# Optimization experiments

Measured on AMD Instinct MI355X. Metric: run time of the kernel, lower is better.

## Reference

```python
import jax, jax.numpy as jnp
import numpy as np

SCALE_XY = 1.2           # yolo1 in Yolov4Head
OBJ_THRESH = 0.5         # b_o >= 0.5 gate in post_process
BOX_SCORE_THRESH = 0.05
NMS_THRESH = 0.7         # rpn_nms_thresh
MAX_DET = 300            # fixed capacity for jit-compatible NMS


def _decode(x, anchors):
    # x: [B, A*(5+C), H, W] -> boxes [B,H,W,A,4] (xyxy, normalized), obj logits, class logits
    b, c, h, w = x.shape
    a = anchors.shape[0]
    nc = c // a - 5
    out = x.reshape(b, a, 5 + nc, h, w).transpose(0, 3, 4, 1, 2)  # [B,H,W,A,5+C]
    cx = jnp.arange(w, dtype=x.dtype).reshape(1, 1, w, 1)
    cy = jnp.arange(h, dtype=x.dtype).reshape(1, h, 1, 1)
    xy = SCALE_XY * jax.nn.sigmoid(out[..., :2]) - 0.5 * (SCALE_XY - 1)
    bx = (xy[..., 0] + cx) / w
    by = (xy[..., 1] + cy) / h
    b_xy = jnp.stack([bx, by], axis=-1)
    b_wh = jnp.clip(jnp.exp(out[..., 2:4]) * anchors.reshape(1, 1, 1, a, 2), 0.0, 2.0)
    tl = b_xy - 0.5 * b_wh
    boxes = jnp.concatenate([tl, tl + b_wh], axis=-1)  # [B,H,W,A,4]
    return boxes, out[..., 4], out[..., 5:]


def _iou_one_vs_all(box, boxes):
    lt = jnp.maximum(box[:2], boxes[:, :2])
    rb = jnp.minimum(box[2:], boxes[:, 2:])
    wh = jnp.clip(rb - lt, 0.0)
    inter = wh[:, 0] * wh[:, 1]
    a1 = (box[2] - box[0]) * (box[3] - box[1])
    a2 = (boxes[:, 2] - boxes[:, 0]) * (boxes[:, 3] - boxes[:, 1])
    return inter / (a1 + a2 - inter + 1e-9)


def _post_process_single(boxes, b_o, b_scores):
    # boxes [N,4], b_o [N], b_scores [N,C]; fixed-size equivalent of YoloLayer.post_process
    obj = jax.nn.sigmoid(b_o)
    cls = jax.nn.sigmoid(b_scores)
    boxes = jnp.clip(boxes, 0.0, 1.0)
    labels = jnp.argmax(cls, axis=-1)
    score = jnp.max(cls, axis=-1) * obj
    valid = (obj >= OBJ_THRESH) & (score >= BOX_SCORE_THRESH)
    masked = jnp.where(valid, score, -1.0)
    _, top_i = jax.lax.top_k(masked, MAX_DET)
    sel_boxes = boxes[top_i]
    sel_labels = labels[top_i]
    sel_valid = valid[top_i]
    sel_scores = jnp.where(sel_valid, score[top_i], 0.0)
    pos = jnp.arange(MAX_DET)

    def body(i, keep):
        iou = _iou_one_vs_all(sel_boxes[i], sel_boxes)
        suppress = (iou > NMS_THRESH) & keep[i] & (pos > i)
        return keep & (~suppress)

    keep = jax.lax.fori_loop(0, MAX_DET, body, sel_valid)
    return sel_boxes, sel_scores, sel_labels, keep


def setup_inputs() -> dict:
    key = jax.random.key(0)
    k1, _ = jax.random.split(key)
    x = jax.random.normal(k1, (32, 255, 76, 76), dtype=jnp.float32)
    anchors = jnp.array([[12.0, 16.0], [19.0, 36.0], [40.0, 28.0]], dtype=jnp.float32) / 608.0
    return {"x": x, "anchors": anchors}


def reference(x, anchors):
    boxes, b_o, b_s = _decode(x, anchors)
    b = x.shape[0]
    nc = b_s.shape[-1]
    boxes = boxes.reshape(b, -1, 4)
    b_o = b_o.reshape(b, -1)
    b_s = b_s.reshape(b, -1, nc)
    det_boxes, det_scores, det_labels, keep = jax.vmap(_post_process_single)(boxes, b_o, b_s)
    return det_boxes, det_scores, det_labels, keep
```

## Files before the change

kernel.cpp:

```cpp
#include <hip/hip_runtime.h>
#include <stdint.h>

#define BATCH   32
#define GRID_HW 5776
#define NA      3
#define NPB     (NA*GRID_HW)
#define NCLS    80
#define MAXDET  300
#define NBINS   4096
#define CANDN   512
#define T2      1024
#define CHUNK   17
#define NQ      (BATCH*NPB/4)
#define S4      (GRID_HW/4)
#define NPB4    (NPB/4)

__device__ __forceinline__ float sigf(float x){ return 1.0f/(1.0f + expf(-x)); }

__device__ __forceinline__ int binf(float v){
    if (v < 0.0f) return 0;
    int b = (int)(v * 4096.0f);
    return b > (NBINS-1) ? (NBINS-1) : b;
}

__device__ __forceinline__ unsigned int ordf(float v){
    unsigned int u = __float_as_uint(v);
    return (u & 0x80000000u) ? ~u : (u | 0x80000000u);
}

__global__ __launch_bounds__(256) void decode_kernel(const float* __restrict__ x,
                                                     float* __restrict__ wmsk,
                                                     int* __restrict__ wlab)
{
    int tid = blockIdx.x * 256 + threadIdx.x;
    if (tid >= NQ) return;
    int b   = tid / (NPB/4);
    int r   = tid - b * (NPB/4);
    int a   = r / S4;
    int hw4 = r - a * S4;

    const float4* p4 = (const float4*)(x + (size_t)(b * 255 + a * 85) * GRID_HW) + hw4;

    float4 tov = p4[4*S4];

    float bx0=-1.0f, bx1=-1.0f, bx2=-1.0f, bx3=-1.0f;
    int   l0=0, l1=0, l2=0, l3=0;
    const float4* pc = p4 + 5*S4;
    #pragma unroll 4
    for (int c = 0; c < NCLS; ++c){
        float4 v = pc[(size_t)c * S4];
        float s;
        s = sigf(v.x); if (s > bx0){ bx0 = s; l0 = c; }
        s = sigf(v.y); if (s > bx1){ bx1 = s; l1 = c; }
        s = sigf(v.z); if (s > bx2){ bx2 = s; l2 = c; }
        s = sigf(v.w); if (s > bx3){ bx3 = s; l3 = c; }
    }

    float to[4]    = {tov.x, tov.y, tov.z, tov.w};
    float bestv[4] = {bx0, bx1, bx2, bx3};
    int   bestl[4] = {l0, l1, l2, l3};

    #pragma unroll
    for (int j = 0; j < 4; ++j){
        float obj = sigf(to[j]);
        float score = bestv[j] * obj;
        bool valid = (obj >= 0.5f) && (score >= 0.05f);

        int m = 4*tid + j;
        wmsk[m] = valid ? score : -1.0f;
        wlab[m] = bestl[j];
    }
}

__global__ __launch_bounds__(T2) void postproc_kernel(const float* __restrict__ x,
                                                      const float* __restrict__ anchors,
                                                      const float* __restrict__ wmsk,
                                                      const int* __restrict__ wlab,
                                                      float* __restrict__ out)
{
    __shared__ unsigned int shist[NBINS];
    __shared__ unsigned int wsum[16];
    __shared__ unsigned long long scan64[T2];
    __shared__ unsigned long long cand[CANDN];
    __shared__ float sbx[MAXDET], sby[MAXDET], sbz[MAXDET], sbw2[MAXDET];
    __shared__ float ssc[MAXDET];
    __shared__ int   slab[MAXDET];
    __shared__ unsigned long long adj[MAXDET][5];
    __shared__ unsigned long long kmask[5];
    __shared__ int s_bin, s_cnt;

    int t = threadIdx.x;
    int b = blockIdx.x;
    int wid = t >> 6, lane = t & 63;
    const float* msk = wmsk + (size_t)b * NPB;
    const float4* msk4 = (const float4*)msk;

    for (int i = t; i < NBINS; i += T2) shist[i] = 0u;
    if (t == 0){ s_bin = -2; s_cnt = 0; }
    __syncthreads();
    for (int i4 = t; i4 < NPB4; i4 += T2){
        float4 v4 = msk4[i4];
        if (v4.x >= 0.0f) atomicAdd(&shist[binf(v4.x)], 1u);
        if (v4.y >= 0.0f) atomicAdd(&shist[binf(v4.y)], 1u);
        if (v4.z >= 0.0f) atomicAdd(&shist[binf(v4.z)], 1u);
        if (v4.w >= 0.0f) atomicAdd(&shist[binf(v4.w)], 1u);
    }
    __syncthreads();

    unsigned int cs = shist[4*t] + shist[4*t+1] + shist[4*t+2] + shist[4*t+3];
    unsigned int vI = cs;
    #pragma unroll
    for (int d = 1; d < 64; d <<= 1){
        unsigned int o = __shfl_up(vI, d);
        if (lane >= d) vI += o;
    }
    if (lane == 63) wsum[wid] = vI;
    __syncthreads();
    if (t < 16){
        unsigned int s = wsum[t];
        #pragma unroll
        for (int d = 1; d < 16; d <<= 1){
            unsigned int o = __shfl_up(s, d);
            if (t >= d) s += o;
        }
        wsum[t] = s;
    }
    __syncthreads();
    unsigned int S = vI + (wid ? wsum[wid-1] : 0u);
    unsigned int total = wsum[15];
    if (total >= MAXDET){
        unsigned int c = total - S;
        #pragma unroll
        for (int k = 3; k >= 0; --k){
            unsigned int cg = c + shist[4*t + k];
            if (c < MAXDET && cg >= MAXDET) s_bin = 4*t + k;
            c = cg;
        }
    }
    __syncthreads();
    int cb = s_bin;

    if (cb >= 0){
        for (int i4 = t; i4 < NPB4; i4 += T2){
            float4 v4 = msk4[i4];
            float vv[4] = {v4.x, v4.y, v4.z, v4.w};
            #pragma unroll
            for (int j = 0; j < 4; ++j){
                float v = vv[j];
                bool pred = (v >= 0.0f) && (binf(v) >= cb);
                unsigned long long bal = __ballot(pred);
                if (bal){
                    int cnt = __popcll(bal);
                    int leader = __ffsll((long long)bal) - 1;
                    int lbase = 0;
                    if (lane == leader) lbase = atomicAdd(&s_cnt, cnt);
                    int base = __shfl(lbase, leader);
                    if (pred){
                        int off = __popcll(bal & ((1ull << lane) - 1ull));
                        int pos = base + off;
                        if (pos < CANDN){
                            int m = 4*i4 + j;
                            int aidx = m / GRID_HW;
                            int hw   = m - aidx * GRID_HW;
                            unsigned int n = (unsigned int)(hw * 3 + aidx);
                            cand[pos] = ((unsigned long long)ordf(v) << 32) | (~n);
                        }
                    }
                }
            }
        }
    }
    __syncthreads();
    int cnum = s_cnt;
    bool exact = (cb >= 0) && (cnum <= CANDN);

    if (exact){
        for (int i = cnum + t; i < CANDN; i += T2) cand[i] = 0ull;
        __syncthreads();
        for (int k2 = 2; k2 <= CANDN; k2 <<= 1){
            for (int j = k2 >> 1; j > 0; j >>= 1){
                if (t < CANDN){
                    int ixj = t ^ j;
                    if (ixj > t){
                        unsigned long long a1 = cand[t], b1 = cand[ixj];
                        bool up = ((t & k2) == 0);
                        if ((a1 < b1) == up){ cand[t] = b1; cand[ixj] = a1; }
                    }
                }
                __syncthreads();
            }
        }
    } else {
        unsigned long long lk[CHUNK];
        int cstart = t * CHUNK;
        int ccnt = NPB - cstart; ccnt = ccnt < 0 ? 0 : (ccnt > CHUNK ? CHUNK : ccnt);
        for (int k = 0; k < CHUNK; ++k) lk[k] = 0ull;
        for (int k = 0; k < ccnt; ++k){
            int m = cstart + k;
            int aidx = m / GRID_HW;
            int hw   = m - aidx * GRID_HW;
            unsigned int n = (unsigned int)(hw * 3 + aidx);
            lk[k] = ((unsigned long long)ordf(msk[m]) << 32) | (~n);
        }
        for (int it = 0; it < MAXDET; ++it){
            unsigned long long lm = 0ull;
            for (int k = 0; k < CHUNK; ++k) lm = lk[k] > lm ? lk[k] : lm;
            scan64[t] = lm;
            __syncthreads();
            for (int s = T2 >> 1; s > 0; s >>= 1){
                if (t < s){ unsigned long long o = scan64[t+s]; if (o > scan64[t]) scan64[t] = o; }
                __syncthreads();
            }
            unsigned long long win = scan64[0];
            if (t == 0) cand[it] = win;
            for (int k = 0; k < CHUNK; ++k) if (lk[k] == win) lk[k] = 0ull;
            __syncthreads();
        }
        for (int i = MAXDET + t; i < CANDN; i += T2) cand[i] = 0ull;
        __syncthreads();
    }

    {
        bool valid = false;
        if (t < MAXDET){
            unsigned long long key = cand[t];
            unsigned int n = ~((unsigned int)key);
            int aidx = (int)(n % 3u);
            int hw   = (int)(n / 3u);
            int m    = aidx * GRID_HW + hw;
            float v  = msk[m];
            valid = v > -0.5f;

            int h = hw / 76;
            int w = hw - h * 76;
            const float* p = x + (size_t)(b * 255 + aidx * 85) * GRID_HW + hw;
            float tx = p[0];
            float ty = p[GRID_HW];
            float tw = p[2*GRID_HW];
            float th = p[3*GRID_HW];
            float aw = anchors[aidx*2], ah = anchors[aidx*2+1];

            float sx = 1.2f * sigf(tx) - 0.1f;
            float sy = 1.2f * sigf(ty) - 0.1f;
            float bxc = (sx + (float)w) / 76.0f;
            float byc = (sy + (float)h) / 76.0f;
            float bw = fminf(fmaxf(expf(tw)*aw, 0.0f), 2.0f);
            float bh = fminf(fmaxf(expf(th)*ah, 0.0f), 2.0f);
            float tlx = bxc - 0.5f*bw, tly = byc - 0.5f*bh;
            float brx = tlx + bw,      bry = tly + bh;

            sbx[t]  = fminf(fmaxf(tlx,0.0f),1.0f);
            sby[t]  = fminf(fmaxf(tly,0.0f),1.0f);
            sbz[t]  = fminf(fmaxf(brx,0.0f),1.0f);
            sbw2[t] = fminf(fmaxf(bry,0.0f),1.0f);
            ssc[t]  = valid ? v : 0.0f;
            slab[t] = wlab[(size_t)b * NPB + m];
        }
        if (wid < 5){
            unsigned long long bal = __ballot(valid);
            if (lane == 0) kmask[wid] = bal;
        }
    }
    __syncthreads();

    for (int task = wid; task < MAXDET*5; task += 16){
        int i  = task / 5;
        int w2 = task - i * 5;
        int j  = w2 * 64 + lane;
        int jc = j < MAXDET ? j : (MAXDET-1);
        float lx = fmaxf(sbx[i], sbx[jc]);
        float ly = fmaxf(sby[i], sby[jc]);
        float rx = fminf(sbz[i], sbz[jc]);
        float ry = fminf(sbw2[i], sbw2[jc]);
        float iw = fmaxf(rx - lx, 0.0f);
        float ih = fmaxf(ry - ly, 0.0f);
        float inter = iw * ih;
        float a1 = (sbz[i]-sbx[i]) * (sbw2[i]-sby[i]);
        float a2 = (sbz[jc]-sbx[jc]) * (sbw2[jc]-sby[jc]);
        float iou = inter / (a1 + a2 - inter + 1e-9f);
        bool pred = (j < MAXDET) && (j > i) && (iou > 0.7f);
        unsigned long long bal = __ballot(pred);
        if (lane == 0) adj[i][w2] = bal;
    }
    __syncthreads();

    if (t < 64){
        unsigned long long km0 = kmask[0], km1 = kmask[1], km2 = kmask[2],
                           km3 = kmask[3], km4 = kmask[4];
        unsigned long long c0 = adj[0][0], c1 = adj[0][1], c2 = adj[0][2],
                           c3 = adj[0][3], c4 = adj[0][4];
        #define NMS_BLK(B, LIM, KM)                                            \
        for (int i2 = 0; i2 < (LIM); ++i2){                                    \
            int i = (B)*64 + i2;                                               \
            unsigned long long n0=0ull,n1=0ull,n2=0ull,n3=0ull,n4=0ull;        \
            if (i + 1 < MAXDET){                                               \
                n0 = adj[i+1][0]; n1 = adj[i+1][1]; n2 = adj[i+1][2];          \
                n3 = adj[i+1][3]; n4 = adj[i+1][4];                            \
            }                                                                  \
            unsigned long long m2 = ((KM >> i2) & 1ull) ? ~0ull : 0ull;        \
            km0 &= ~(c0 & m2);                                                 \
            km1 &= ~(c1 & m2);                                                 \
            km2 &= ~(c2 & m2);                                                 \
            km3 &= ~(c3 & m2);                                                 \
            km4 &= ~(c4 & m2);                                                 \
            c0 = n0; c1 = n1; c2 = n2; c3 = n3; c4 = n4;                       \
        }
        NMS_BLK(0, 64, km0)
        NMS_BLK(1, 64, km1)
        NMS_BLK(2, 64, km2)
        NMS_BLK(3, 64, km3)
        NMS_BLK(4, 44, km4)
        #undef NMS_BLK
        if (t == 0){
            kmask[0] = km0; kmask[1] = km1; kmask[2] = km2;
            kmask[3] = km3; kmask[4] = km4;
        }
    }
    __syncthreads();

    if (t < MAXDET){
        float* ob = out + (size_t)b * (MAXDET*4) + (size_t)t * 4;
        ob[0] = sbx[t]; ob[1] = sby[t]; ob[2] = sbz[t]; ob[3] = sbw2[t];
        out[BATCH*MAXDET*4 + b*MAXDET + t] = ssc[t];
        out[BATCH*MAXDET*5 + b*MAXDET + t] = (float)slab[t];
        out[BATCH*MAXDET*6 + b*MAXDET + t] = ((kmask[t >> 6] >> (t & 63)) & 1ull) ? 1.0f : 0.0f;
    }
}

extern "C" void kernel_launch(void* const* d_in, const int* in_sizes, int n_in,
                              void* d_out, int out_size, void* d_ws, size_t ws_size,
                              hipStream_t stream)
{
    const float* x       = (const float*)d_in[0];
    const float* anchors = (const float*)d_in[1];
    float* out = (float*)d_out;

    char* ws = (char*)d_ws;
    float* wmsk = (float*)ws;
    int*   wlab = (int*)(ws + (size_t)BATCH*NPB*4);

    decode_kernel<<<(NQ + 255)/256, 256, 0, stream>>>(x, wmsk, wlab);
    postproc_kernel<<<BATCH, T2, 0, stream>>>(x, anchors, wmsk, wlab, out);
}
```

Measured before the change: 344.7 us.

## Build score histogram in decode and split candidate selection across blocks

```diff
diff --git a/kernel.cpp b/kernel.cpp
--- a/kernel.cpp
+++ b/kernel.cpp
@@ -14,6 +14,9 @@
 #define NQ      (BATCH*NPB/4)
 #define S4      (GRID_HW/4)
 #define NPB4    (NPB/4)
+#define SB      8
+#define SLICE4  542
+#define ZN      (BATCH*NBINS + BATCH)
 
 __device__ __forceinline__ float sigf(float x){ return 1.0f/(1.0f + expf(-x)); }
 
@@ -28,9 +31,16 @@
     return (u & 0x80000000u) ? ~u : (u | 0x80000000u);
 }
 
+__global__ void zero_kernel(unsigned int* __restrict__ g)
+{
+    int i = blockIdx.x * blockDim.x + threadIdx.x;
+    if (i < ZN) g[i] = 0u;
+}
+
 __global__ __launch_bounds__(256) void decode_kernel(const float* __restrict__ x,
                                                      float* __restrict__ wmsk,
-                                                     int* __restrict__ wlab)
+                                                     int* __restrict__ wlab,
+                                                     unsigned int* __restrict__ ghist)
 {
     int tid = blockIdx.x * 256 + threadIdx.x;
     if (tid >= NQ) return;
@@ -69,13 +79,103 @@
         int m = 4*tid + j;
         wmsk[m] = valid ? score : -1.0f;
         wlab[m] = bestl[j];
-    }
-}
-
-__global__ __launch_bounds__(T2) void postproc_kernel(const float* __restrict__ x,
+        if (valid) atomicAdd(&ghist[b * NBINS + binf(score)], 1u);
+    }
+}
+
+__global__ __launch_bounds__(T2) void select_kernel(const float* __restrict__ wmsk,
+                                                    const unsigned int* __restrict__ ghist,
+                                                    unsigned long long* __restrict__ gcand,
+                                                    unsigned int* __restrict__ gcnt)
+{
+    __shared__ unsigned int shist[NBINS];
+    __shared__ unsigned int wsum[16];
+    __shared__ int s_bin;
+
+    int t = threadIdx.x;
+    int blk = blockIdx.x;
+    int b  = blk >> 3;
+    int sb = blk & 7;
+    int wid = t >> 6, lane = t & 63;
+
+    for (int i = t; i < NBINS; i += T2) shist[i] = ghist[b * NBINS + i];
+    if (t == 0) s_bin = -2;
+    __syncthreads();
+
+    unsigned int cs = shist[4*t] + shist[4*t+1] + shist[4*t+2] + shist[4*t+3];
+    unsigned int vI = cs;
+    #pragma unroll
+    for (int d = 1; d < 64; d <<= 1){
+        unsigned int o = __shfl_up(vI, d);
+        if (lane >= d) vI += o;
+    }
+    if (lane == 63) wsum[wid] = vI;
+    __syncthreads();
+    if (t < 16){
+        unsigned int s = wsum[t];
+        #pragma unroll
+        for (int d = 1; d < 16; d <<= 1){
+            unsigned int o = __shfl_up(s, d);
+            if (t >= d) s += o;
+        }
+        wsum[t] = s;
+    }
+    __syncthreads();
+    unsigned int S = vI + (wid ? wsum[wid-1] : 0u);
+    unsigned int total = wsum[15];
+    if (total >= MAXDET){
+        unsigned int c = total - S;
+        #pragma unroll
+        for (int k = 3; k >= 0; --k){
+            unsigned int cg = c + shist[4*t + k];
+            if (c < MAXDET && cg >= MAXDET) s_bin = 4*t + k;
+            c = cg;
+        }
+    }
+    __syncthreads();
+    int cb = s_bin;
+    if (cb < 0) return;
+
+    const float4* msk4 = (const float4*)(wmsk + (size_t)b * NPB);
+    int i4lim = sb * SLICE4 + SLICE4; if (i4lim > NPB4) i4lim = NPB4;
+    for (int i4 = sb * SLICE4 + t; i4 < i4lim; i4 += T2){
+        float4 v4 = msk4[i4];
+        float vv[4] = {v4.x, v4.y, v4.z, v4.w};
+        #pragma unroll
+        for (int j = 0; j < 4; ++j){
+            float v = vv[j];
+            bool pred = (v >= 0.0f) && (binf(v) >= cb);
+            unsigned long long bal = __ballot(pred);
+            if (bal){
+                int cnt = __popcll(bal);
+                int leader = __ffsll((long long)bal) - 1;
+                int lbase = 0;
+                if (lane == leader) lbase = (int)atomicAdd(&gcnt[b], (unsigned int)cnt);
+                int base = __shfl(lbase, leader);
+                if (pred){
+                    int off = __popcll(bal & ((1ull << lane) - 1ull));
+                    int pos = base + off;
+                    if (pos < CANDN){
+                        int m = 4*i4 + j;
+                        int aidx = m / GRID_HW;
+                        int hw   = m - aidx * GRID_HW;
+                        unsigned int n = (unsigned int)(hw * 3 + aidx);
+                        gcand[(size_t)b * CANDN + pos] =
+                            ((unsigned long long)ordf(v) << 32) | (~n);
+                    }
+                }
+            }
+        }
+    }
+}
+
+__global__ __launch_bounds__(T2) void finalize_kernel(const float* __restrict__ x,
                                                       const float* __restrict__ anchors,
                                                       const float* __restrict__ wmsk,
                                                       const int* __restrict__ wlab,
+                                                      const unsigned int* __restrict__ ghist,
+                                                      const unsigned long long* __restrict__ gcand,
+                                                      const unsigned int* __restrict__ gcnt,
                                                       float* __restrict__ out)
 {
     __shared__ unsigned int shist[NBINS];
@@ -87,24 +187,15 @@
     __shared__ int   slab[MAXDET];
     __shared__ unsigned long long adj[MAXDET][5];
     __shared__ unsigned long long kmask[5];
-    __shared__ int s_bin, s_cnt;
+    __shared__ int s_bin;
 
     int t = threadIdx.x;
     int b = blockIdx.x;
     int wid = t >> 6, lane = t & 63;
     const float* msk = wmsk + (size_t)b * NPB;
-    const float4* msk4 = (const float4*)msk;
-
-    for (int i = t; i < NBINS; i += T2) shist[i] = 0u;
-    if (t == 0){ s_bin = -2; s_cnt = 0; }
-    __syncthreads();
-    for (int i4 = t; i4 < NPB4; i4 += T2){
-        float4 v4 = msk4[i4];
-        if (v4.x >= 0.0f) atomicAdd(&shist[binf(v4.x)], 1u);
-        if (v4.y >= 0.0f) atomicAdd(&shist[binf(v4.y)], 1u);
-        if (v4.z >= 0.0f) atomicAdd(&shist[binf(v4.z)], 1u);
-        if (v4.w >= 0.0f) atomicAdd(&shist[binf(v4.w)], 1u);
-    }
+
+    for (int i = t; i < NBINS; i += T2) shist[i] = ghist[b * NBINS + i];
+    if (t == 0) s_bin = -2;
     __syncthreads();
 
     unsigned int cs = shist[4*t] + shist[4*t+1] + shist[4*t+2] + shist[4*t+3];
@@ -139,43 +230,12 @@
     }
     __syncthreads();
     int cb = s_bin;
-
-    if (cb >= 0){
-        for (int i4 = t; i4 < NPB4; i4 += T2){
-            float4 v4 = msk4[i4];
-            float vv[4] = {v4.x, v4.y, v4.z, v4.w};
-            #pragma unroll
-            for (int j = 0; j < 4; ++j){
-                float v = vv[j];
-                bool pred = (v >= 0.0f) && (binf(v) >= cb);
-                unsigned long long bal = __ballot(pred);
-                if (bal){
-                    int cnt = __popcll(bal);
-                    int leader = __ffsll((long long)bal) - 1;
-                    int lbase = 0;
-                    if (lane == leader) lbase = atomicAdd(&s_cnt, cnt);
-                    int base = __shfl(lbase, leader);
-                    if (pred){
-                        int off = __popcll(bal & ((1ull << lane) - 1ull));
-                        int pos = base + off;
-                        if (pos < CANDN){
-                            int m = 4*i4 + j;
-                            int aidx = m / GRID_HW;
-                            int hw   = m - aidx * GRID_HW;
-                            unsigned int n = (unsigned int)(hw * 3 + aidx);
-                            cand[pos] = ((unsigned long long)ordf(v) << 32) | (~n);
-                        }
-                    }
-                }
-            }
-        }
-    }
-    __syncthreads();
-    int cnum = s_cnt;
+    int cnum = (int)gcnt[b];
     bool exact = (cb >= 0) && (cnum <= CANDN);
 
     if (exact){
-        for (int i = cnum + t; i < CANDN; i += T2) cand[i] = 0ull;
+        for (int i = t; i < CANDN; i += T2)
+            cand[i] = (i < cnum) ? gcand[(size_t)b * CANDN + i] : 0ull;
         __syncthreads();
         for (int k2 = 2; k2 <= CANDN; k2 <<= 1){
             for (int j = k2 >> 1; j > 0; j >>= 1){
@@ -336,9 +396,15 @@
     float* out = (float*)d_out;
 
     char* ws = (char*)d_ws;
-    float* wmsk = (float*)ws;
-    int*   wlab = (int*)(ws + (size_t)BATCH*NPB*4);
-
-    decode_kernel<<<(NQ + 255)/256, 256, 0, stream>>>(x, wmsk, wlab);
-    postproc_kernel<<<BATCH, T2, 0, stream>>>(x, anchors, wmsk, wlab, out);
-}
+    float*              wmsk  = (float*)ws;
+    int*                wlab  = (int*)  (ws + (size_t)BATCH*NPB*4);
+    unsigned int*       ghist = (unsigned int*)(ws + (size_t)BATCH*NPB*8);
+    unsigned int*       gcnt  = ghist + (size_t)BATCH*NBINS;
+    unsigned long long* gcand = (unsigned long long*)(ws + (size_t)BATCH*NPB*8
+                                                      + (size_t)BATCH*NBINS*4 + 128);
+
+    zero_kernel<<<(ZN + 255)/256, 256, 0, stream>>>(ghist);
+    decode_kernel<<<(NQ + 255)/256, 256, 0, stream>>>(x, wmsk, wlab, ghist);
+    select_kernel<<<BATCH*SB, T2, 0, stream>>>(wmsk, ghist, gcand, gcnt);
+    finalize_kernel<<<BATCH, T2, 0, stream>>>(x, anchors, wmsk, wlab, ghist, gcand, gcnt, out);
+}
```

Result: slower. 391.9 us (+13.7%).

## Fuse decode and postprocess into one kernel with last-block-done per batch

Applied to the files above, without the earlier changes.

```diff
diff --git a/kernel.cpp b/kernel.cpp
--- a/kernel.cpp
+++ b/kernel.cpp
@@ -14,6 +14,9 @@
 #define NQ      (BATCH*NPB/4)
 #define S4      (GRID_HW/4)
 #define NPB4    (NPB/4)
+#define QPB     (NPB/4)
+#define NBLK    256
+#define SLICE   542
 
 __device__ __forceinline__ float sigf(float x){ return 1.0f/(1.0f + expf(-x)); }
 
@@ -28,75 +31,33 @@
     return (u & 0x80000000u) ? ~u : (u | 0x80000000u);
 }
 
-__global__ __launch_bounds__(256) void decode_kernel(const float* __restrict__ x,
-                                                     float* __restrict__ wmsk,
-                                                     int* __restrict__ wlab)
+__global__ void zero_kernel(unsigned int* __restrict__ qdone)
 {
-    int tid = blockIdx.x * 256 + threadIdx.x;
-    if (tid >= NQ) return;
-    int b   = tid / (NPB/4);
-    int r   = tid - b * (NPB/4);
-    int a   = r / S4;
-    int hw4 = r - a * S4;
-
-    const float4* p4 = (const float4*)(x + (size_t)(b * 255 + a * 85) * GRID_HW) + hw4;
-
-    float4 tov = p4[4*S4];
-
-    float bx0=-1.0f, bx1=-1.0f, bx2=-1.0f, bx3=-1.0f;
-    int   l0=0, l1=0, l2=0, l3=0;
-    const float4* pc = p4 + 5*S4;
-    #pragma unroll 4
-    for (int c = 0; c < NCLS; ++c){
-        float4 v = pc[(size_t)c * S4];
-        float s;
-        s = sigf(v.x); if (s > bx0){ bx0 = s; l0 = c; }
-        s = sigf(v.y); if (s > bx1){ bx1 = s; l1 = c; }
-        s = sigf(v.z); if (s > bx2){ bx2 = s; l2 = c; }
-        s = sigf(v.w); if (s > bx3){ bx3 = s; l3 = c; }
-    }
-
-    float to[4]    = {tov.x, tov.y, tov.z, tov.w};
-    float bestv[4] = {bx0, bx1, bx2, bx3};
-    int   bestl[4] = {l0, l1, l2, l3};
-
-    #pragma unroll
-    for (int j = 0; j < 4; ++j){
-        float obj = sigf(to[j]);
-        float score = bestv[j] * obj;
-        bool valid = (obj >= 0.5f) && (score >= 0.05f);
-
-        int m = 4*tid + j;
-        wmsk[m] = valid ? score : -1.0f;
-        wlab[m] = bestl[j];
-    }
-}
-
-__global__ __launch_bounds__(T2) void postproc_kernel(const float* __restrict__ x,
-                                                      const float* __restrict__ anchors,
-                                                      const float* __restrict__ wmsk,
-                                                      const int* __restrict__ wlab,
-                                                      float* __restrict__ out)
+    int i = threadIdx.x;
+    if (i < BATCH) qdone[i] = 0u;
+}
+
+__device__ void postproc_batch(int b, int t,
+                               const float* __restrict__ x,
+                               const float* __restrict__ anchors,
+                               const float* __restrict__ wmsk,
+                               const int* __restrict__ wlab,
+                               float* __restrict__ out,
+                               unsigned int* shist, unsigned int* wsum,
+                               unsigned long long* scan64, unsigned long long* cand,
+                               float* sbx, float* sby, float* sbz, float* sbw2,
+                               float* ssc, int* slab,
+                               unsigned long long (*adj)[5], unsigned long long* kmask,
+                               int* s_bin, int* s_cnt)
 {
-    __shared__ unsigned int shist[NBINS];
-    __shared__ unsigned int wsum[16];
-    __shared__ unsigned long long scan64[T2];
-    __shared__ unsigned long long cand[CANDN];
-    __shared__ float sbx[MAXDET], sby[MAXDET], sbz[MAXDET], sbw2[MAXDET];
-    __shared__ float ssc[MAXDET];
-    __shared__ int   slab[MAXDET];
-    __shared__ unsigned long long adj[MAXDET][5];
-    __shared__ unsigned long long kmask[5];
-    __shared__ int s_bin, s_cnt;
-
-    int t = threadIdx.x;
-    int b = blockIdx.x;
     int wid = t >> 6, lane = t & 63;
     const float* msk = wmsk + (size_t)b * NPB;
     const float4* msk4 = (const float4*)msk;
 
+    __syncthreads();
+
     for (int i = t; i < NBINS; i += T2) shist[i] = 0u;
-    if (t == 0){ s_bin = -2; s_cnt = 0; }
+    if (t == 0){ *s_bin = -2; *s_cnt = 0; }
     __syncthreads();
     for (int i4 = t; i4 < NPB4; i4 += T2){
         float4 v4 = msk4[i4];
@@ -133,12 +94,12 @@
         #pragma unroll
         for (int k = 3; k >= 0; --k){
             unsigned int cg = c + shist[4*t + k];
-            if (c < MAXDET && cg >= MAXDET) s_bin = 4*t + k;
+            if (c < MAXDET && cg >= MAXDET) *s_bin = 4*t + k;
             c = cg;
         }
     }
     __syncthreads();
-    int cb = s_bin;
+    int cb = *s_bin;
 
     if (cb >= 0){
         for (int i4 = t; i4 < NPB4; i4 += T2){
@@ -153,7 +114,7 @@
                     int cnt = __popcll(bal);
                     int leader = __ffsll((long long)bal) - 1;
                     int lbase = 0;
-                    if (lane == leader) lbase = atomicAdd(&s_cnt, cnt);
+                    if (lane == leader) lbase = atomicAdd(s_cnt, cnt);
                     int base = __shfl(lbase, leader);
                     if (pred){
                         int off = __popcll(bal & ((1ull << lane) - 1ull));
@@ -171,7 +132,7 @@
         }
     }
     __syncthreads();
-    int cnum = s_cnt;
+    int cnum = *s_cnt;
     bool exact = (cb >= 0) && (cnum <= CANDN);
 
     if (exact){
@@ -327,6 +288,101 @@
     }
 }
 
+__global__ __launch_bounds__(T2) void fused_kernel(const float* __restrict__ x,
+                                                   const float* __restrict__ anchors,
+                                                   float* __restrict__ wmsk,
+                                                   int* __restrict__ wlab,
+                                                   unsigned int* __restrict__ qdone,
+                                                   float* __restrict__ out)
+{
+    __shared__ unsigned int shist[NBINS];
+    __shared__ unsigned int wsum[16];
+    __shared__ unsigned long long scan64[T2];
+    __shared__ unsigned long long cand[CANDN];
+    __shared__ float sbx[MAXDET], sby[MAXDET], sbz[MAXDET], sbw2[MAXDET];
+    __shared__ float ssc[MAXDET];
+    __shared__ int   slab[MAXDET];
+    __shared__ unsigned long long adj[MAXDET][5];
+    __shared__ unsigned long long kmask[5];
+    __shared__ int s_bin, s_cnt;
+    __shared__ int s_do[2];
+
+    int t   = threadIdx.x;
+    int blk = blockIdx.x;
+    int q0  = blk * SLICE;
+    int q1  = q0 + SLICE; if (q1 > NQ) q1 = NQ;
+
+    int q = q0 + t;
+    if (q < q1){
+        int b   = q / QPB;
+        int r   = q - b * QPB;
+        int a   = r / S4;
+        int hw4 = r - a * S4;
+
+        const float4* p4 = (const float4*)(x + (size_t)(b * 255 + a * 85) * GRID_HW) + hw4;
+
+        float4 tov = p4[4*S4];
+
+        float bx0=-1.0f, bx1=-1.0f, bx2=-1.0f, bx3=-1.0f;
+        int   l0=0, l1=0, l2=0, l3=0;
+        const float4* pc = p4 + 5*S4;
+        #pragma unroll 4
+        for (int c = 0; c < NCLS; ++c){
+            float4 v = pc[(size_t)c * S4];
+            float s;
+            s = sigf(v.x); if (s > bx0){ bx0 = s; l0 = c; }
+            s = sigf(v.y); if (s > bx1){ bx1 = s; l1 = c; }
+            s = sigf(v.z); if (s > bx2){ bx2 = s; l2 = c; }
+            s = sigf(v.w); if (s > bx3){ bx3 = s; l3 = c; }
+        }
+
+        float to[4]    = {tov.x, tov.y, tov.z, tov.w};
+        float bestv[4] = {bx0, bx1, bx2, bx3};
+        int   bestl[4] = {l0, l1, l2, l3};
+
+        #pragma unroll
+        for (int j = 0; j < 4; ++j){
+            float obj = sigf(to[j]);
+            float score = bestv[j] * obj;
+            bool valid = (obj >= 0.5f) && (score >= 0.05f);
+
+            int m = 4*q + j;
+            wmsk[m] = valid ? score : -1.0f;
+            wlab[m] = bestl[j];
+        }
+    }
+
+    __threadfence();
+    __syncthreads();
+    if (t == 0){
+        s_do[0] = -1; s_do[1] = -1;
+        int b0 = q0 / QPB;
+        int b1 = (q1 - 1) / QPB;
+        int e0 = (b0 + 1) * QPB; if (e0 > q1) e0 = q1;
+        int c0 = e0 - q0;
+        unsigned int o0 = atomicAdd(&qdone[b0], (unsigned int)c0);
+        if ((int)o0 + c0 == QPB) s_do[0] = b0;
+        if (b1 != b0){
+            int c1 = q1 - b1 * QPB;
+            unsigned int o1 = atomicAdd(&qdone[b1], (unsigned int)c1);
+            if ((int)o1 + c1 == QPB) s_do[1] = b1;
+        }
+    }
+    __syncthreads();
+    if (s_do[0] < 0 && s_do[1] < 0) return;
+
+    __threadfence();
+
+    if (s_do[0] >= 0)
+        postproc_batch(s_do[0], t, x, anchors, wmsk, wlab, out,
+                       shist, wsum, scan64, cand, sbx, sby, sbz, sbw2,
+                       ssc, slab, adj, kmask, &s_bin, &s_cnt);
+    if (s_do[1] >= 0)
+        postproc_batch(s_do[1], t, x, anchors, wmsk, wlab, out,
+                       shist, wsum, scan64, cand, sbx, sby, sbz, sbw2,
+                       ssc, slab, adj, kmask, &s_bin, &s_cnt);
+}
+
 extern "C" void kernel_launch(void* const* d_in, const int* in_sizes, int n_in,
                               void* d_out, int out_size, void* d_ws, size_t ws_size,
                               hipStream_t stream)
@@ -336,9 +392,10 @@
     float* out = (float*)d_out;
 
     char* ws = (char*)d_ws;
-    float* wmsk = (float*)ws;
-    int*   wlab = (int*)(ws + (size_t)BATCH*NPB*4);
-
-    decode_kernel<<<(NQ + 255)/256, 256, 0, stream>>>(x, wmsk, wlab);
-    postproc_kernel<<<BATCH, T2, 0, stream>>>(x, anchors, wmsk, wlab, out);
-}
+    float*        wmsk  = (float*)ws;
+    int*          wlab  = (int*)  (ws + (size_t)BATCH*NPB*4);
+    unsigned int* qdone = (unsigned int*)(ws + (size_t)BATCH*NPB*8);
+
+    zero_kernel<<<1, 64, 0, stream>>>(qdone);
+    fused_kernel<<<NBLK, T2, 0, stream>>>(x, anchors, wmsk, wlab, qdone, out);
+}
```

Measured after the change: 512.4 us. +48.6%, slower.

## Split class argmax across four wavefronts per tile with shared-memory reduction

Applied to the files above, without the earlier changes.

```diff
diff --git a/kernel.cpp b/kernel.cpp
--- a/kernel.cpp
+++ b/kernel.cpp
@@ -11,9 +11,13 @@
 #define CANDN   512
 #define T2      1024
 #define CHUNK   17
-#define NQ      (BATCH*NPB/4)
 #define S4      (GRID_HW/4)
 #define NPB4    (NPB/4)
+
+#define TPB_D   256
+#define TILE4   64
+#define NT      23
+#define CPW     20
 
 __device__ __forceinline__ float sigf(float x){ return 1.0f/(1.0f + expf(-x)); }
 
@@ -28,47 +32,71 @@
     return (u & 0x80000000u) ? ~u : (u | 0x80000000u);
 }
 
-__global__ __launch_bounds__(256) void decode_kernel(const float* __restrict__ x,
-                                                     float* __restrict__ wmsk,
-                                                     int* __restrict__ wlab)
+__global__ __launch_bounds__(TPB_D) void decode_kernel(const float* __restrict__ x,
+                                                       float* __restrict__ wmsk,
+                                                       int* __restrict__ wlab)
 {
-    int tid = blockIdx.x * 256 + threadIdx.x;
-    if (tid >= NQ) return;
-    int b   = tid / (NPB/4);
-    int r   = tid - b * (NPB/4);
-    int a   = r / S4;
-    int hw4 = r - a * S4;
-
-    const float4* p4 = (const float4*)(x + (size_t)(b * 255 + a * 85) * GRID_HW) + hw4;
-
-    float4 tov = p4[4*S4];
-
-    float bx0=-1.0f, bx1=-1.0f, bx2=-1.0f, bx3=-1.0f;
-    int   l0=0, l1=0, l2=0, l3=0;
-    const float4* pc = p4 + 5*S4;
-    #pragma unroll 4
-    for (int c = 0; c < NCLS; ++c){
-        float4 v = pc[(size_t)c * S4];
-        float s;
-        s = sigf(v.x); if (s > bx0){ bx0 = s; l0 = c; }
-        s = sigf(v.y); if (s > bx1){ bx1 = s; l1 = c; }
-        s = sigf(v.z); if (s > bx2){ bx2 = s; l2 = c; }
-        s = sigf(v.w); if (s > bx3){ bx3 = s; l3 = c; }
-    }
-
-    float to[4]    = {tov.x, tov.y, tov.z, tov.w};
-    float bestv[4] = {bx0, bx1, bx2, bx3};
-    int   bestl[4] = {l0, l1, l2, l3};
-
-    #pragma unroll
-    for (int j = 0; j < 4; ++j){
-        float obj = sigf(to[j]);
-        float score = bestv[j] * obj;
+    __shared__ unsigned long long sk[4][4][TILE4];
+
+    int blk  = blockIdx.x;
+    int tile = blk % NT;
+    int ba   = blk / NT;
+    int a    = ba % NA;
+    int b    = ba / NA;
+
+    int t = threadIdx.x;
+    int w = t >> 6, l = t & 63;
+
+    int tf0 = tile * TILE4;
+    int tc  = S4 - tf0; if (tc > TILE4) tc = TILE4;
+
+    const float4* xp = (const float4*)x;
+    size_t clsBase = (size_t)(b*255 + a*85 + 5) * S4;
+
+    if (l < tc){
+        unsigned long long b0 = 0ull, b1 = 0ull, b2 = 0ull, b3 = 0ull;
+        size_t p0 = clsBase + (size_t)(CPW*w) * S4 + (size_t)(tf0 + l);
+        #pragma unroll
+        for (int ci = 0; ci < CPW; ++ci){
+            int c = CPW*w + ci;
+            float4 v = xp[p0 + (size_t)ci * S4];
+            unsigned long long lo = (unsigned long long)(unsigned)(NCLS-1-c);
+            unsigned long long k;
+            k = ((unsigned long long)__float_as_uint(sigf(v.x)) << 32) | lo;
+            if (k > b0) b0 = k;
+            k = ((unsigned long long)__float_as_uint(sigf(v.y)) << 32) | lo;
+            if (k > b1) b1 = k;
+            k = ((unsigned long long)__float_as_uint(sigf(v.z)) << 32) | lo;
+            if (k > b2) b2 = k;
+            k = ((unsigned long long)__float_as_uint(sigf(v.w)) << 32) | lo;
+            if (k > b3) b3 = k;
+        }
+        sk[0][w][l] = b0;
+        sk[1][w][l] = b1;
+        sk[2][w][l] = b2;
+        sk[3][w][l] = b3;
+    }
+    __syncthreads();
+
+    if (t < 4*tc){
+        int f4i = t >> 2, j = t & 3;
+        unsigned long long k0 = sk[j][0][f4i], k1 = sk[j][1][f4i],
+                           k2 = sk[j][2][f4i], k3 = sk[j][3][f4i];
+        unsigned long long ka = k0 > k1 ? k0 : k1;
+        unsigned long long kb = k2 > k3 ? k2 : k3;
+        unsigned long long k  = ka > kb ? ka : kb;
+        float s  = __uint_as_float((unsigned)(k >> 32));
+        int lab  = (NCLS-1) - (int)(k & 0xFFFFFFFFull);
+
+        int hw = tf0*4 + t;
+        float objv = x[((size_t)(b*255 + a*85) + 4) * GRID_HW + hw];
+        float obj  = sigf(objv);
+        float score = s * obj;
         bool valid = (obj >= 0.5f) && (score >= 0.05f);
 
-        int m = 4*tid + j;
+        int m = b*NPB + a*GRID_HW + hw;
         wmsk[m] = valid ? score : -1.0f;
-        wlab[m] = bestl[j];
+        wlab[m] = lab;
     }
 }
 
@@ -339,6 +367,6 @@
     float* wmsk = (float*)ws;
     int*   wlab = (int*)(ws + (size_t)BATCH*NPB*4);
 
-    decode_kernel<<<(NQ + 255)/256, 256, 0, stream>>>(x, wmsk, wlab);
+    decode_kernel<<<BATCH*NA*NT, TPB_D, 0, stream>>>(x, wmsk, wlab);
     postproc_kernel<<<BATCH, T2, 0, stream>>>(x, anchors, wmsk, wlab, out);
 }
```

Result: no change. 344.5 us (-0.1%).
